# Kernel tuning notes

Hardware: AMD Instinct MI355X
Metric: run time of the kernel (lower is better)

## Reference

```python
import jax, jax.numpy as jnp
import numpy as np

B, N, D = 4, 4096, 2048
H = 16          # heads
KH = 16         # k_per_head (must equal heads for the view to be valid)
DK = D // H     # 128


def setup_inputs() -> dict:
    key = jax.random.key(0)
    kx, kq, kk, kv, ko = jax.random.split(key, 5)
    s = 1.0 / np.sqrt(D).astype(np.float32)  # ~torch Linear init scale
    return {
        "x": jax.random.normal(kx, (B, N, D), jnp.float32),
        "Wq": jax.random.normal(kq, (D, D), jnp.float32) * s,
        "Wk": jax.random.normal(kk, (D, D), jnp.float32) * s,
        "Wv": jax.random.normal(kv, (D, D), jnp.float32) * s,
        "Wo": jax.random.normal(ko, (D, D), jnp.float32) * s,
    }


def reference(x, Wq, Wk, Wv, Wo):
    b, n, d = x.shape
    # QKV projections (bias-free Linear; weight stored as (in, out))
    q = (x @ Wq).reshape(b, n, H, DK)    # (B,N,H,DK)
    k = (x @ Wk).reshape(b, n, KH, DK)   # (B,N,KH,DK)
    v = (x @ Wv).reshape(b, n, KH, DK)   # (B,N,KH,DK)
    # softmax-free matmul chain, batched per token: (H,DK)@(DK,KH)@(KH,DK)
    scores = jnp.einsum("bnhd,bnkd->bnhk", q, k)   # (B,N,H,KH)
    o = jnp.einsum("bnhk,bnkd->bnhd", scores, v)   # (B,N,H,DK)
    return o.reshape(b, n, d) @ Wo                 # (B,N,D)
```

## Files before the change

### kernel.cpp

```cpp
#include <hip/hip_runtime.h>
#include <hip/hip_bf16.h>

#define BB 4
#define NN 4096
#define DD 2048
#define HH 16
#define DK 128
#define MTOK (BB * NN)
#define QKVW (3 * DD)

typedef __bf16 bf16x8 __attribute__((ext_vector_type(8)));
typedef __bf16 bf16x4 __attribute__((ext_vector_type(4)));
typedef float f32x4 __attribute__((ext_vector_type(4)));

__device__ __forceinline__ void gload16(const __bf16* g, __bf16* lds_wave_uniform_base) {
    __builtin_amdgcn_global_load_lds(
        (const __attribute__((address_space(1))) void*)g,
        (__attribute__((address_space(3))) void*)lds_wave_uniform_base,
        16, 0, 0);
}

__global__ __launch_bounds__(256) void xconv_kernel(const float* __restrict__ X,
                                                    __bf16* __restrict__ Xb, int n4) {
    int i = blockIdx.x * blockDim.x + threadIdx.x;
    if (i < n4) {
        float4 v = reinterpret_cast<const float4*>(X)[i];
        bf16x4 o;
        o[0] = (__bf16)v.x; o[1] = (__bf16)v.y; o[2] = (__bf16)v.z; o[3] = (__bf16)v.w;
        reinterpret_cast<bf16x4*>(Xb)[i] = o;
    }
}

__global__ __launch_bounds__(256) void wconv_kernel(const float* __restrict__ W0,
                                                    const float* __restrict__ W1,
                                                    const float* __restrict__ W2,
                                                    const float* __restrict__ W3,
                                                    __bf16* __restrict__ Wcat,
                                                    __bf16* __restrict__ Wo_t) {
    __shared__ float tile[32][33];
    const int w = blockIdx.z;
    const float* W = (w == 0) ? W0 : (w == 1) ? W1 : (w == 2) ? W2 : W3;
    __bf16* dst = (w < 3) ? (Wcat + (size_t)w * DD * DD) : Wo_t;
    const int tx = threadIdx.x, ty = threadIdx.y;
    const int n0 = blockIdx.x * 32, k0 = blockIdx.y * 32;
#pragma unroll
    for (int j = 0; j < 32; j += 8)
        tile[ty + j][tx] = W[(size_t)(k0 + ty + j) * DD + n0 + tx];
    __syncthreads();
#pragma unroll
    for (int j = 0; j < 32; j += 8)
        dst[(size_t)(n0 + ty + j) * DD + k0 + tx] = (__bf16)tile[tx][ty + j];
}

template <typename OutT>
__global__ __launch_bounds__(512, 2) void gemm256(const __bf16* __restrict__ A, int lda,
                                                  const __bf16* __restrict__ Bt, int ldb,
                                                  OutT* __restrict__ C, int ldc, int K) {
    __shared__ __align__(16) __bf16 lds[2][4][8192];
    const int NT = K >> 6;

    const int tid = threadIdx.x;
    const int wave = tid >> 6, lane = tid & 63;
    const int wm = wave >> 2, wn = wave & 3;

    const int nbx = gridDim.x;
    const int nwg = nbx * gridDim.y;
    int flat = blockIdx.y * nbx + blockIdx.x;
    flat = (flat & 7) * (nwg >> 3) + (flat >> 3);
    const size_t blockM = (size_t)(flat / nbx) * 256;
    const size_t blockN = (size_t)(flat % nbx) * 256;

    const int kel = ((((lane >> 1) ^ (lane >> 5)) & 1) << 4) + ((lane & 1) << 3);
    const __bf16* sA = A + (blockM + (size_t)(lane >> 2)) * lda + kel;
    const __bf16* sB = Bt + (blockN + (size_t)(lane >> 2)) * ldb + kel;

    const int ldsOff = (lane & 15) * 64 + (((lane >> 4) * 16) ^ (((lane >> 3) & 1) << 5));
    const int aOff = wm * 8192 + ldsOff;
    const int bOff = wn * 4096 + ldsOff;

#define STAGE_A(t, khc)                                                                   \
    do {                                                                                  \
        const int _k = (t) * 64 + (khc) * 32;                                             \
        gload16(sA + (size_t)(wave * 32) * lda + _k,                                      \
                &lds[(t) & 1][(khc)][wave * 1024]);                                       \
        gload16(sA + (size_t)(wave * 32 + 16) * lda + _k,                                 \
                &lds[(t) & 1][(khc)][wave * 1024 + 512]);                                 \
    } while (0)
#define STAGE_B(t, khc)                                                                   \
    do {                                                                                  \
        const int _k = (t) * 64 + (khc) * 32;                                             \
        gload16(sB + (size_t)(wave * 32) * ldb + _k,                                      \
                &lds[(t) & 1][2 + (khc)][wave * 1024]);                                   \
        gload16(sB + (size_t)(wave * 32 + 16) * ldb + _k,                                 \
                &lds[(t) & 1][2 + (khc)][wave * 1024 + 512]);                             \
    } while (0)

    f32x4 acc[8][4] = {};

    STAGE_A(0, 0); STAGE_B(0, 0); STAGE_A(0, 1); STAGE_B(0, 1);
    STAGE_B(1, 0); STAGE_B(1, 1); STAGE_A(1, 0);
    asm volatile("s_waitcnt vmcnt(6)" ::: "memory");
    asm volatile("s_barrier" ::: "memory");

#pragma unroll 2
    for (int T = 0; T < NT; ++T) {
        const int b = T & 1;
        bf16x8 bk0[4], bk1[4];

        {
            bf16x8 af[4];
            const char* Ag = (const char*)&lds[b][0][0];
            const char* Bg = (const char*)&lds[b][2][0];
#pragma unroll
            for (int mi = 0; mi < 4; ++mi)
                af[mi] = *(const bf16x8*)(Ag + aOff + mi * 1024);
#pragma unroll
            for (int ni = 0; ni < 4; ++ni)
                bk0[ni] = *(const bf16x8*)(Bg + bOff + ni * 1024);
            if (T + 1 < NT) STAGE_A(T + 1, 1);
            asm volatile("s_barrier" ::: "memory");
            __builtin_amdgcn_sched_barrier(0);
            __builtin_amdgcn_s_setprio(1);
#pragma unroll
            for (int mi = 0; mi < 4; ++mi)
#pragma unroll
                for (int ni = 0; ni < 4; ++ni)
                    acc[mi][ni] = __builtin_amdgcn_mfma_f32_16x16x32_bf16(
                        af[mi], bk0[ni], acc[mi][ni], 0, 0, 0);
            __builtin_amdgcn_sched_barrier(0);
            __builtin_amdgcn_s_setprio(0);
            asm volatile("s_barrier" ::: "memory");
        }

        {
            bf16x8 af[4];
            const char* Ag = (const char*)&lds[b][1][0];
            const char* Bg = (const char*)&lds[b][3][0];
#pragma unroll
            for (int mi = 0; mi < 4; ++mi)
                af[mi] = *(const bf16x8*)(Ag + aOff + mi * 1024);
#pragma unroll
            for (int ni = 0; ni < 4; ++ni)
                bk1[ni] = *(const bf16x8*)(Bg + bOff + ni * 1024);
            if (T + 2 < NT) STAGE_B(T + 2, 0);
            asm volatile("s_barrier" ::: "memory");
            __builtin_amdgcn_sched_barrier(0);
            __builtin_amdgcn_s_setprio(1);
#pragma unroll
            for (int mi = 0; mi < 4; ++mi)
#pragma unroll
                for (int ni = 0; ni < 4; ++ni)
                    acc[mi][ni] = __builtin_amdgcn_mfma_f32_16x16x32_bf16(
                        af[mi], bk1[ni], acc[mi][ni], 0, 0, 0);
            __builtin_amdgcn_sched_barrier(0);
            __builtin_amdgcn_s_setprio(0);
            asm volatile("s_barrier" ::: "memory");
        }

        {
            bf16x8 af[4];
            const char* Ag = (const char*)&lds[b][0][0];
#pragma unroll
            for (int mi = 0; mi < 4; ++mi)
                af[mi] = *(const bf16x8*)(Ag + aOff + 4096 + mi * 1024);
            if (T + 2 < NT) STAGE_B(T + 2, 1);
            asm volatile("s_barrier" ::: "memory");
            __builtin_amdgcn_sched_barrier(0);
            __builtin_amdgcn_s_setprio(1);
#pragma unroll
            for (int mi = 0; mi < 4; ++mi)
#pragma unroll
                for (int ni = 0; ni < 4; ++ni)
                    acc[4 + mi][ni] = __builtin_amdgcn_mfma_f32_16x16x32_bf16(
                        af[mi], bk0[ni], acc[4 + mi][ni], 0, 0, 0);
            __builtin_amdgcn_sched_barrier(0);
            __builtin_amdgcn_s_setprio(0);
            asm volatile("s_barrier" ::: "memory");
        }

        {
            bf16x8 af[4];
            const char* Ag = (const char*)&lds[b][1][0];
#pragma unroll
            for (int mi = 0; mi < 4; ++mi)
                af[mi] = *(const bf16x8*)(Ag + aOff + 4096 + mi * 1024);
            if (T + 2 < NT) STAGE_A(T + 2, 0);
            asm volatile("s_barrier" ::: "memory");
            __builtin_amdgcn_sched_barrier(0);
            __builtin_amdgcn_s_setprio(1);
#pragma unroll
            for (int mi = 0; mi < 4; ++mi)
#pragma unroll
                for (int ni = 0; ni < 4; ++ni)
                    acc[4 + mi][ni] = __builtin_amdgcn_mfma_f32_16x16x32_bf16(
                        af[mi], bk1[ni], acc[4 + mi][ni], 0, 0, 0);
            __builtin_amdgcn_sched_barrier(0);
            __builtin_amdgcn_s_setprio(0);
            if (T + 2 < NT) asm volatile("s_waitcnt vmcnt(6)" ::: "memory");
            else            asm volatile("s_waitcnt vmcnt(0)" ::: "memory");
            asm volatile("s_barrier" ::: "memory");
        }
    }
#undef STAGE_A
#undef STAGE_B

    const int rEp = (lane >> 4) * 4;
    const int cEp = lane & 15;
#pragma unroll
    for (int mi = 0; mi < 8; ++mi) {
        const size_t row0 = blockM + wm * 128 + mi * 16 + rEp;
#pragma unroll
        for (int ni = 0; ni < 4; ++ni) {
            const size_t col = blockN + wn * 64 + ni * 16 + cEp;
#pragma unroll
            for (int r = 0; r < 4; ++r)
                C[(row0 + r) * (size_t)ldc + col] = (OutT)acc[mi][ni][r];
        }
    }
}

__global__ __launch_bounds__(256) void attn_kernel(const __bf16* __restrict__ qkv,
                                                   __bf16* __restrict__ Ob) {
    __shared__ float sc[4][16][17];
    const int tid = threadIdx.x;
    const int wave = tid >> 6;
    const int lane = tid & 63;
    const int t = lane & 15;
    const int quad = lane >> 4;
    const size_t token = (size_t)blockIdx.x * 4 + wave;
    const __bf16* row = qkv + token * QKVW;
    __bf16* orow = Ob + token * DD;

    f32x4 s = (f32x4){0.f, 0.f, 0.f, 0.f};
#pragma unroll
    for (int ks = 0; ks < 4; ++ks) {
        bf16x8 a = *reinterpret_cast<const bf16x8*>(row + t * DK + ks * 32 + quad * 8);
        bf16x8 b = *reinterpret_cast<const bf16x8*>(row + DD + t * DK + ks * 32 + quad * 8);
        s = __builtin_amdgcn_mfma_f32_16x16x32_bf16(a, b, s, 0, 0, 0);
    }
#pragma unroll
    for (int i = 0; i < 4; ++i) sc[wave][quad * 4 + i][t] = s[i];
    __syncthreads();

    const int d0 = t * 8;
    float oa[4][8];
#pragma unroll
    for (int i = 0; i < 4; ++i)
#pragma unroll
        for (int e = 0; e < 8; ++e) oa[i][e] = 0.f;

#pragma unroll
    for (int j = 0; j < 16; ++j) {
        bf16x8 v8 = *reinterpret_cast<const bf16x8*>(row + 2 * DD + j * DK + d0);
        float vf[8];
#pragma unroll
        for (int e = 0; e < 8; ++e) vf[e] = (float)v8[e];
#pragma unroll
        for (int i = 0; i < 4; ++i) {
            const float sj = sc[wave][quad + 4 * i][j];
#pragma unroll
            for (int e = 0; e < 8; ++e) oa[i][e] += sj * vf[e];
        }
    }
#pragma unroll
    for (int i = 0; i < 4; ++i) {
        bf16x8 o8;
#pragma unroll
        for (int e = 0; e < 8; ++e) o8[e] = (__bf16)oa[i][e];
        *reinterpret_cast<bf16x8*>(orow + (quad + 4 * i) * DK + d0) = o8;
    }
}

extern "C" void kernel_launch(void* const* d_in, const int* in_sizes, int n_in,
                              void* d_out, int out_size, void* d_ws, size_t ws_size,
                              hipStream_t stream) {
    const float* X  = (const float*)d_in[0];
    const float* Wq = (const float*)d_in[1];
    const float* Wk = (const float*)d_in[2];
    const float* Wv = (const float*)d_in[3];
    const float* Wo = (const float*)d_in[4];
    float* out = (float*)d_out;

    char* ws = (char*)d_ws;
    __bf16* Wcat = (__bf16*)ws;
    __bf16* Wo_t = (__bf16*)(ws + (size_t)3 * DD * DD * 2);
    __bf16* Xb   = (__bf16*)(ws + (size_t)4 * DD * DD * 2);
    __bf16* QKV  = (__bf16*)(ws + (size_t)4 * DD * DD * 2 + (size_t)MTOK * DD * 2);
    __bf16* Ob   = Xb;

    const int n4 = MTOK * DD / 4;
    xconv_kernel<<<(n4 + 255) / 256, 256, 0, stream>>>(X, Xb, n4);

    wconv_kernel<<<dim3(DD / 32, DD / 32, 4), dim3(32, 8), 0, stream>>>(
        Wq, Wk, Wv, Wo, Wcat, Wo_t);

    gemm256<__bf16><<<dim3(QKVW / 256, MTOK / 256), 512, 0, stream>>>(
        Xb, DD, Wcat, DD, QKV, QKVW, DD);

    attn_kernel<<<MTOK / 4, 256, 0, stream>>>(QKV, Ob);

    gemm256<float><<<dim3(DD / 256, MTOK / 256), 512, 0, stream>>>(
        Ob, DD, Wo_t, DD, out, DD, DD);
}
```

Before: 799.8 us.

## Hoist LDS fragment loads ahead and cut barriers in the GEMM main loop

Restructures the bf16 MFMA main loop so that all A and B fragments for the first two K-halves are read from LDS up front. The a2/a3 fragments are read early as well. Partial s_waitcnt lgkmcnt waits replace the barrier that preceded each MFMA phase. This overlaps LDS read latency with MFMA issue and removes one workgroup barrier per phase. In exchange it holds more fragment registers live, which may lower occupancy or cause spills. It also depends on the lgkmcnt counts and the remaining barriers being enough to order LDS reads against later async global-to-LDS stages.

```diff
diff --git a/kernel.cpp b/kernel.cpp
--- a/kernel.cpp
+++ b/kernel.cpp
@@ -105,101 +105,83 @@
 #pragma unroll 2
     for (int T = 0; T < NT; ++T) {
         const int b = T & 1;
-        bf16x8 bk0[4], bk1[4];
-
-        {
-            bf16x8 af[4];
-            const char* Ag = (const char*)&lds[b][0][0];
-            const char* Bg = (const char*)&lds[b][2][0];
-#pragma unroll
-            for (int mi = 0; mi < 4; ++mi)
-                af[mi] = *(const bf16x8*)(Ag + aOff + mi * 1024);
-#pragma unroll
-            for (int ni = 0; ni < 4; ++ni)
-                bk0[ni] = *(const bf16x8*)(Bg + bOff + ni * 1024);
-            if (T + 1 < NT) STAGE_A(T + 1, 1);
-            asm volatile("s_barrier" ::: "memory");
-            __builtin_amdgcn_sched_barrier(0);
-            __builtin_amdgcn_s_setprio(1);
-#pragma unroll
-            for (int mi = 0; mi < 4; ++mi)
-#pragma unroll
-                for (int ni = 0; ni < 4; ++ni)
-                    acc[mi][ni] = __builtin_amdgcn_mfma_f32_16x16x32_bf16(
-                        af[mi], bk0[ni], acc[mi][ni], 0, 0, 0);
-            __builtin_amdgcn_sched_barrier(0);
-            __builtin_amdgcn_s_setprio(0);
-            asm volatile("s_barrier" ::: "memory");
-        }
-
-        {
-            bf16x8 af[4];
-            const char* Ag = (const char*)&lds[b][1][0];
-            const char* Bg = (const char*)&lds[b][3][0];
-#pragma unroll
-            for (int mi = 0; mi < 4; ++mi)
-                af[mi] = *(const bf16x8*)(Ag + aOff + mi * 1024);
-#pragma unroll
-            for (int ni = 0; ni < 4; ++ni)
-                bk1[ni] = *(const bf16x8*)(Bg + bOff + ni * 1024);
-            if (T + 2 < NT) STAGE_B(T + 2, 0);
-            asm volatile("s_barrier" ::: "memory");
-            __builtin_amdgcn_sched_barrier(0);
-            __builtin_amdgcn_s_setprio(1);
-#pragma unroll
-            for (int mi = 0; mi < 4; ++mi)
-#pragma unroll
-                for (int ni = 0; ni < 4; ++ni)
-                    acc[mi][ni] = __builtin_amdgcn_mfma_f32_16x16x32_bf16(
-                        af[mi], bk1[ni], acc[mi][ni], 0, 0, 0);
-            __builtin_amdgcn_sched_barrier(0);
-            __builtin_amdgcn_s_setprio(0);
-            asm volatile("s_barrier" ::: "memory");
-        }
-
-        {
-            bf16x8 af[4];
-            const char* Ag = (const char*)&lds[b][0][0];
-#pragma unroll
-            for (int mi = 0; mi < 4; ++mi)
-                af[mi] = *(const bf16x8*)(Ag + aOff + 4096 + mi * 1024);
-            if (T + 2 < NT) STAGE_B(T + 2, 1);
-            asm volatile("s_barrier" ::: "memory");
-            __builtin_amdgcn_sched_barrier(0);
-            __builtin_amdgcn_s_setprio(1);
-#pragma unroll
-            for (int mi = 0; mi < 4; ++mi)
-#pragma unroll
-                for (int ni = 0; ni < 4; ++ni)
-                    acc[4 + mi][ni] = __builtin_amdgcn_mfma_f32_16x16x32_bf16(
-                        af[mi], bk0[ni], acc[4 + mi][ni], 0, 0, 0);
-            __builtin_amdgcn_sched_barrier(0);
-            __builtin_amdgcn_s_setprio(0);
-            asm volatile("s_barrier" ::: "memory");
-        }
-
-        {
-            bf16x8 af[4];
-            const char* Ag = (const char*)&lds[b][1][0];
-#pragma unroll
-            for (int mi = 0; mi < 4; ++mi)
-                af[mi] = *(const bf16x8*)(Ag + aOff + 4096 + mi * 1024);
-            if (T + 2 < NT) STAGE_A(T + 2, 0);
-            asm volatile("s_barrier" ::: "memory");
-            __builtin_amdgcn_sched_barrier(0);
-            __builtin_amdgcn_s_setprio(1);
-#pragma unroll
-            for (int mi = 0; mi < 4; ++mi)
-#pragma unroll
-                for (int ni = 0; ni < 4; ++ni)
-                    acc[4 + mi][ni] = __builtin_amdgcn_mfma_f32_16x16x32_bf16(
-                        af[mi], bk1[ni], acc[4 + mi][ni], 0, 0, 0);
-            __builtin_amdgcn_sched_barrier(0);
-            __builtin_amdgcn_s_setprio(0);
-            if (T + 2 < NT) asm volatile("s_waitcnt vmcnt(6)" ::: "memory");
-            else            asm volatile("s_waitcnt vmcnt(0)" ::: "memory");
-            asm volatile("s_barrier" ::: "memory");
-        }
+        const char* Ag0 = (const char*)&lds[b][0][0];
+        const char* Ag1 = (const char*)&lds[b][1][0];
+        const char* Bg0 = (const char*)&lds[b][2][0];
+        const char* Bg1 = (const char*)&lds[b][3][0];
+        bf16x8 a0[4], a1[4], a2[4], a3[4], b0[4], b1[4];
+
+#pragma unroll
+        for (int mi = 0; mi < 4; ++mi) a0[mi] = *(const bf16x8*)(Ag0 + aOff + mi * 1024);
+#pragma unroll
+        for (int ni = 0; ni < 4; ++ni) b0[ni] = *(const bf16x8*)(Bg0 + bOff + ni * 1024);
+#pragma unroll
+        for (int mi = 0; mi < 4; ++mi) a1[mi] = *(const bf16x8*)(Ag1 + aOff + mi * 1024);
+#pragma unroll
+        for (int ni = 0; ni < 4; ++ni) b1[ni] = *(const bf16x8*)(Bg1 + bOff + ni * 1024);
+        if (T + 1 < NT) STAGE_A(T + 1, 1);
+        asm volatile("s_waitcnt lgkmcnt(8)" ::: "memory");
+        __builtin_amdgcn_sched_barrier(0);
+        __builtin_amdgcn_s_setprio(1);
+#pragma unroll
+        for (int mi = 0; mi < 4; ++mi)
+#pragma unroll
+            for (int ni = 0; ni < 4; ++ni)
+                acc[mi][ni] = __builtin_amdgcn_mfma_f32_16x16x32_bf16(
+                    a0[mi], b0[ni], acc[mi][ni], 0, 0, 0);
+        __builtin_amdgcn_sched_barrier(0);
+        __builtin_amdgcn_s_setprio(0);
+        asm volatile("s_barrier" ::: "memory");
+
+#pragma unroll
+        for (int mi = 0; mi < 4; ++mi)
+            a2[mi] = *(const bf16x8*)(Ag0 + aOff + 4096 + mi * 1024);
+#pragma unroll
+        for (int mi = 0; mi < 4; ++mi)
+            a3[mi] = *(const bf16x8*)(Ag1 + aOff + 4096 + mi * 1024);
+        if (T + 2 < NT) STAGE_B(T + 2, 0);
+        asm volatile("s_waitcnt lgkmcnt(8)" ::: "memory");
+        __builtin_amdgcn_sched_barrier(0);
+        __builtin_amdgcn_s_setprio(1);
+#pragma unroll
+        for (int mi = 0; mi < 4; ++mi)
+#pragma unroll
+            for (int ni = 0; ni < 4; ++ni)
+                acc[mi][ni] = __builtin_amdgcn_mfma_f32_16x16x32_bf16(
+                    a1[mi], b1[ni], acc[mi][ni], 0, 0, 0);
+        __builtin_amdgcn_sched_barrier(0);
+        __builtin_amdgcn_s_setprio(0);
+        asm volatile("s_barrier" ::: "memory");
+
+        if (T + 2 < NT) STAGE_B(T + 2, 1);
+        asm volatile("s_waitcnt lgkmcnt(4)" ::: "memory");
+        __builtin_amdgcn_sched_barrier(0);
+        __builtin_amdgcn_s_setprio(1);
+#pragma unroll
+        for (int mi = 0; mi < 4; ++mi)
+#pragma unroll
+            for (int ni = 0; ni < 4; ++ni)
+                acc[4 + mi][ni] = __builtin_amdgcn_mfma_f32_16x16x32_bf16(
+                    a2[mi], b0[ni], acc[4 + mi][ni], 0, 0, 0);
+        __builtin_amdgcn_sched_barrier(0);
+        __builtin_amdgcn_s_setprio(0);
+        asm volatile("s_barrier" ::: "memory");
+
+        if (T + 2 < NT) STAGE_A(T + 2, 0);
+        asm volatile("s_waitcnt lgkmcnt(0)" ::: "memory");
+        __builtin_amdgcn_sched_barrier(0);
+        __builtin_amdgcn_s_setprio(1);
+#pragma unroll
+        for (int mi = 0; mi < 4; ++mi)
+#pragma unroll
+            for (int ni = 0; ni < 4; ++ni)
+                acc[4 + mi][ni] = __builtin_amdgcn_mfma_f32_16x16x32_bf16(
+                    a3[mi], b1[ni], acc[4 + mi][ni], 0, 0, 0);
+        __builtin_amdgcn_sched_barrier(0);
+        __builtin_amdgcn_s_setprio(0);
+        if (T + 2 < NT) asm volatile("s_waitcnt vmcnt(6)" ::: "memory");
+        else            asm volatile("s_waitcnt vmcnt(0)" ::: "memory");
+        asm volatile("s_barrier" ::: "memory");
     }
 #undef STAGE_A
 #undef STAGE_B
```

Result: faster. 781.5 us (-2.3%).
